# Performance work log

Hardware: AMD Instinct MI355X
Metric: run time of the kernel (lower is better)

Reference implementation:

```python
import jax, jax.numpy as jnp
import numpy as np

NUM_HEADS = 8
NSCALE = 2  # len(sr_ratio) + 1 with sr_ratio=[2.0]


def setup_inputs() -> dict:
    key = jax.random.key(0)
    ks = jax.random.split(key, 12)
    B, Nq, Np, C, n_up, N_all = 16, 1024, 1024, 512, 2048, 4096
    s = C ** -0.5  # keep attention logits in a sane range
    return {
        "query": jax.random.normal(ks[0], (Nq, B, C), jnp.float32),
        "key": jax.random.normal(ks[1], (Np, B, C), jnp.float32),
        "key_pos": jax.random.uniform(ks[2], (B, Np, 3), jnp.float32),
        "xyz_all": jax.random.uniform(ks[3], (B, N_all, 3), jnp.float32),
        "xyz_upsample": jax.random.uniform(ks[4], (B, n_up, 3), jnp.float32),
        "Wq": jax.random.normal(ks[5], (C, C), jnp.float32) * s,
        "Wkv1": jax.random.normal(ks[6], (C, C), jnp.float32) * s,
        "Wkv2": jax.random.normal(ks[7], (C, C), jnp.float32) * s,
        "fp_w": jax.random.normal(ks[8], (C, C), jnp.float32) * s,
        "fp_b": jnp.zeros((C,), jnp.float32),
        "proj_w": jax.random.normal(ks[9], (C, C), jnp.float32) * s,
        "proj_b": jnp.zeros((C,), jnp.float32),
    }


def _fp_upsample(xyz_up, key_pos, key_feats, fp_w, fp_b):
    """PointnetFPModuleUpSample: 3-NN inverse-distance feature interpolation
    from Np known points (key_pos) onto n_up target points, followed by a
    pointwise MLP (1x1 conv, BN folded) + ReLU.
    key_feats: (Np, B, C) -> returns (B, n_up, C)."""
    d2 = jnp.sum((xyz_up[:, :, None, :] - key_pos[:, None, :, :]) ** 2, axis=-1)  # (B, n, Np)
    negd, idx = jax.lax.top_k(-d2, 3)  # 3 nearest neighbors, (B, n, 3)
    w = 1.0 / (-negd + 1e-8)
    w = w / jnp.sum(w, axis=-1, keepdims=True)
    feats = jnp.transpose(key_feats, (1, 0, 2))  # (B, Np, C)
    g = jnp.take_along_axis(feats[:, None, :, :], idx[..., None], axis=2)  # (B, n, 3, C)
    interp = jnp.sum(g * w[..., None], axis=2)  # (B, n, C)
    return jax.nn.relu(interp @ fp_w.T + fp_b)


def reference(query, key, key_pos, xyz_all, xyz_upsample,
              Wq, Wkv1, Wkv2, fp_w, fp_b, proj_w, proj_b):
    Np, B, C = key.shape
    Nq = query.shape[0]
    H = NUM_HEADS
    nh = H // NSCALE  # heads per scale group
    hd = C // H
    scale = hd ** -0.5

    # NOTE: torch reshapes (N,B,C) -> (B,N,...) WITHOUT permuting first; we
    # replicate the identical row-major reshape for bit-faithful structure.
    q = (query @ Wq.T).reshape(B, Nq, H, hd).transpose(0, 2, 1, 3)  # (B,H,Nq,hd)

    def attend(qs, kv):
        k, v = kv[0], kv[1]
        a = jax.nn.softmax(jnp.einsum('bhqd,bhkd->bhqk', qs, k) * scale, axis=-1)
        o = jnp.einsum('bhqk,bhkd->bhqd', a, v)
        return o.transpose(0, 2, 1, 3).reshape(B, Nq, nh * hd)

    # scale 1: full-resolution keys
    kv1 = (key @ Wkv1.T).reshape(B, -1, 2, nh, hd).transpose(2, 0, 3, 1, 4)
    x1 = attend(q[:, :nh], kv1)

    # scale 2: FP-upsampled keys (sr_ratio=2.0 -> 2*base_np points)
    key2 = _fp_upsample(xyz_upsample, key_pos, key, fp_w, fp_b)  # (B, n, C)
    key2_nbc = key2.transpose(1, 0, 2)  # (n, B, C), matches permute(2,0,1) of (B,C,n)
    kv2 = (key2_nbc @ Wkv2.T).reshape(B, -1, 2, nh, hd).transpose(2, 0, 3, 1, 4)
    x2 = attend(q[:, nh:], kv2)

    x = jnp.concatenate([x1, x2], axis=-1) @ proj_w.T + proj_b  # (B, Nq, C)
    return x.transpose(1, 0, 2)  # (Nq, B, C)
```

## Files before the change

### kernel.cpp

```cpp
#include <hip/hip_runtime.h>
#include <cstdint>
#include <cstddef>

#define CD   512
#define BDIM 16
#define NQ   1024
#define NP   1024
#define NUP  2048

typedef unsigned short u16;
typedef short short8 __attribute__((ext_vector_type(8)));
typedef float f32x4  __attribute__((ext_vector_type(4)));
typedef float f32x16 __attribute__((ext_vector_type(16)));
typedef uint32_t u32x4 __attribute__((ext_vector_type(4)));

#define GLOAD16(g, l) __builtin_amdgcn_global_load_lds( \
    (const __attribute__((address_space(1))) void*)(g), \
    (__attribute__((address_space(3))) void*)(l), 16, 0, 0)

__device__ __forceinline__ u16 rne_bf16(float x) {
  uint32_t u = __float_as_uint(x);
  return (u16)((u + 0x7fffu + ((u >> 16) & 1u)) >> 16);
}
__device__ __forceinline__ float bf2f(u16 v) {
  return __uint_as_float(((uint32_t)v) << 16);
}

__global__ __launch_bounds__(256) void prep_kernel(
    const float* __restrict__ query, u16* __restrict__ Qa,
    const float* __restrict__ key, u16* __restrict__ Ka,
    const float* __restrict__ Wq, const float* __restrict__ Wkv1,
    const float* __restrict__ projw, const float* __restrict__ fpw,
    const float* __restrict__ wkv2, u16* __restrict__ Wq2,
    u16* __restrict__ Wkv12, u16* __restrict__ proj2,
    u16* __restrict__ fpwb, u16* __restrict__ wkv2b,
    const float* __restrict__ key_pos, const float* __restrict__ xyz_up,
    int* __restrict__ idx_out, float* __restrict__ w_out)
{
  const int bx = blockIdx.x;
  const int tid = threadIdx.x;
  if (bx < 8832) {
    const float* in; u16* out; float scl = 1.0f; long u;
    if (bx < 8192) {
      in = (bx < 4096) ? query : key;
      out = (bx < 4096) ? Qa : Ka;
      u = (long)(bx & 4095) * 256 + tid;
    } else {
      const int job = (bx - 8192) >> 7;
      in  = (job == 0) ? Wq  : (job == 1) ? Wkv1  : (job == 2) ? projw : (job == 3) ? fpw  : wkv2;
      out = (job == 0) ? Wq2 : (job == 1) ? Wkv12 : (job == 2) ? proj2 : (job == 3) ? fpwb : wkv2b;
      if (job == 0) scl = 0.18033688011112042f;
      u = (long)((bx - 8192) & 127) * 256 + tid;
    }
    const float* ip = in + u * 8;
    float v[8];
    *(float4*)&v[0] = *(const float4*)ip;
    *(float4*)&v[4] = *(const float4*)(ip + 4);
    short8 o;
#pragma unroll
    for (int i = 0; i < 8; ++i) o[i] = (short)rne_bf16(v[i] * scl);
    *(short8*)(out + u * 8) = o;
    return;
  }
  __shared__ __align__(16) float4 kp4[NP];
  const int kb = bx - 8832;
  const int b = kb >> 7;
  const int n0 = (kb & 127) * 16;
  const float* kpb = key_pos + (long)b * NP * 3;
#pragma unroll
  for (int s = 0; s < 4; ++s) {
    const int t = s * 256 + tid;
    kp4[t] = make_float4(kpb[t * 3], kpb[t * 3 + 1], kpb[t * 3 + 2], 0.0f);
  }
  __syncthreads();
  const int sc = tid & 15, pt = tid >> 4;
  const int n = n0 + pt;
  const float ux = xyz_up[(b * NUP + n) * 3 + 0];
  const float uy = xyz_up[(b * NUP + n) * 3 + 1];
  const float uz = xyz_up[(b * NUP + n) * 3 + 2];
  float e0 = 3.4e38f, e1 = 3.4e38f, e2 = 3.4e38f;
  int j0 = 0, j1 = 0, j2 = 0;
  for (int it = 0; it < 64; ++it) {
    const int j = it * 16 + sc;
    const float4 kv = kp4[j];
    const float dx = ux - kv.x, dy = uy - kv.y, dz = uz - kv.z;
    const float dd = dx * dx + dy * dy + dz * dz;
    if (dd < e2) {
      if (dd < e1) {
        e2 = e1; j2 = j1;
        if (dd < e0) { e1 = e0; j1 = j0; e0 = dd; j0 = j; }
        else         { e1 = dd; j1 = j; }
      } else { e2 = dd; j2 = j; }
    }
  }
#pragma unroll
  for (int ms = 1; ms <= 8; ms <<= 1) {
    const float pd0 = __shfl_xor(e0, ms), pd1 = __shfl_xor(e1, ms), pd2 = __shfl_xor(e2, ms);
    const int   pi0 = __shfl_xor(j0, ms), pi1 = __shfl_xor(j1, ms), pi2 = __shfl_xor(j2, ms);
    float cd[3] = {pd0, pd1, pd2};
    int   ci[3] = {pi0, pi1, pi2};
#pragma unroll
    for (int t = 0; t < 3; ++t) {
      const float dd = cd[t]; const int jj = ci[t];
      if (dd < e2 || (dd == e2 && jj < j2)) {
        if (dd < e1 || (dd == e1 && jj < j1)) {
          e2 = e1; j2 = j1;
          if (dd < e0 || (dd == e0 && jj < j0)) { e1 = e0; j1 = j0; e0 = dd; j0 = jj; }
          else                                  { e1 = dd; j1 = jj; }
        } else { e2 = dd; j2 = jj; }
      }
    }
  }
  if (sc == 0) {
    const float w0 = 1.0f / (e0 + 1e-8f);
    const float w1 = 1.0f / (e1 + 1e-8f);
    const float w2 = 1.0f / (e2 + 1e-8f);
    const float inv = 1.0f / ((w0 + w1) + w2);
    const long r = (long)b * NUP + n;
    idx_out[r * 3 + 0] = j0; idx_out[r * 3 + 1] = j1; idx_out[r * 3 + 2] = j2;
    w_out[r * 3 + 0] = w0 * inv; w_out[r * 3 + 1] = w1 * inv; w_out[r * 3 + 2] = w2 * inv;
  }
}

template<int AMODE, int OMODE, int KE, int NKT>
__device__ __forceinline__ void gemm_body64(
    u16* __restrict__ As, u16* __restrict__ Ws,
    const u16* __restrict__ A, const u16* __restrict__ W,
    const float* __restrict__ bias, void* __restrict__ outv,
    u16* __restrict__ Vt, const int m0, const int n0)
{
  const int tid = threadIdx.x;
  const int lane = tid & 63, wv = tid >> 6;
  const int rch = tid & 7;

  f32x4 acc[4][4];
#pragma unroll
  for (int mi = 0; mi < 4; ++mi)
#pragma unroll
    for (int ni = 0; ni < 4; ++ni)
#pragma unroll
      for (int r = 0; r < 4; ++r) acc[mi][ni][r] = 0.0f;

  const long rowb = (long)KE * 2;
  const char* gA[4]; const char* gW[4];
#pragma unroll
  for (int s = 0; s < 4; ++s) {
    const int row = s * 32 + (tid >> 3);
    const int gm = m0 + row;
    const long arow = (AMODE == 0) ? (long)gm : (long)(gm & 15) * 2048 + (gm >> 4);
    const int kb0 = (rch ^ (row & 7)) << 4;
    gA[s] = (const char*)A + arow * rowb + kb0;
    gW[s] = (const char*)W + (long)(n0 + row) * rowb + kb0;
  }
  const int wr = (wv >> 1) * 64, wc = (wv & 1) * 64;
  const int g = lane >> 4, cl = lane & 15;

  for (int kt = 0; kt < KE / 64; ++kt) {
#pragma unroll
    for (int s = 0; s < 4; ++s) {
      GLOAD16(gA[s], (char*)As + (s * 256 + tid) * 16);
      GLOAD16(gW[s], (char*)Ws + (s * 256 + tid) * 16);
      gA[s] += 128; gW[s] += 128;
    }
    __syncthreads();
#pragma unroll
    for (int kb = 0; kb < 2; ++kb) {
      short8 af[4], bf[4];
#pragma unroll
      for (int i = 0; i < 4; ++i) {
        const int ra = wr + i * 16 + cl;
        af[i] = *(const short8*)((const char*)As + ra * 128
                 + ((kb * 64 + g * 16) ^ ((ra & 7) << 4)));
        const int rb = wc + i * 16 + cl;
        bf[i] = *(const short8*)((const char*)Ws + rb * 128
                 + ((kb * 64 + g * 16) ^ ((rb & 7) << 4)));
      }
#pragma unroll
      for (int mi = 0; mi < 4; ++mi)
#pragma unroll
        for (int ni = 0; ni < 4; ++ni)
          acc[mi][ni] = __builtin_amdgcn_mfma_f32_16x16x32_bf16(af[mi], bf[ni], acc[mi][ni], 0, 0, 0);
    }
    __syncthreads();
  }

  if constexpr (OMODE == 3) {
    u16* T = As;
#pragma unroll
    for (int ni = 0; ni < 4; ++ni) {
      const int n = wc + ni * 16 + cl;
      const int swz = (n & 15) << 4;
      const int rb2 = n * 256;
#pragma unroll
      for (int mi = 0; mi < 4; ++mi) {
        uint32_t lo, hi;
        asm("v_cvt_pk_bf16_f32 %0, %1, %2" : "=v"(lo) : "v"(acc[mi][ni][0]), "v"(acc[mi][ni][1]));
        asm("v_cvt_pk_bf16_f32 %0, %1, %2" : "=v"(hi) : "v"(acc[mi][ni][2]), "v"(acc[mi][ni][3]));
        const int m2 = 2 * (wr + mi * 16 + g * 4);
        uint2 pk; pk.x = lo; pk.y = hi;
        *(uint2*)((char*)T + rb2 + (m2 ^ swz)) = pk;
      }
    }
    __syncthreads();
    const int nl = tid >> 1, mh = tid & 1;
    const int v = (n0 - 256) + nl;
    const int hh = v >> 6, dd = v & 63;
    const int bq = m0 / NKT;
    const int p0 = (m0 & (NKT - 1)) + mh * 64;
    u16* dst = Vt + ((size_t)((bq * 4 + hh) * 64 + dd)) * NKT + p0;
    const int swz = (nl & 15) << 4;
#pragma unroll
    for (int j = 0; j < 8; ++j) {
      const int m2 = mh * 128 + j * 16;
      const short8 val = *(const short8*)((const char*)T + nl * 256 + (m2 ^ swz));
      *(short8*)(dst + j * 8) = val;
    }
    return;
  } else {
#pragma unroll
    for (int mi = 0; mi < 4; ++mi)
#pragma unroll
      for (int ni = 0; ni < 4; ++ni)
#pragma unroll
        for (int r = 0; r < 4; ++r) {
          const int gm = m0 + wr + mi * 16 + g * 4 + r;
          const int gn = n0 + wc + ni * 16 + cl;
          float vv = acc[mi][ni][r];
          if (OMODE == 0) {
            ((u16*)outv)[(long)gm * 512 + gn] = rne_bf16(vv);
          } else if (OMODE == 1) {
            vv = fmaxf(vv + bias[gn], 0.0f);
            ((u16*)outv)[(long)gm * 512 + gn] = rne_bf16(vv);
          } else {
            vv += bias[gn];
            ((float*)outv)[((long)(gm & 1023) * BDIM + (gm >> 10)) * 512 + gn] = vv;
          }
        }
  }
}

template<int AMODE, int OMODE, int KE>
__global__ __launch_bounds__(256) void gemm_one(
    const u16* __restrict__ A, const u16* __restrict__ W,
    const float* __restrict__ bias, void* __restrict__ outv)
{
  __shared__ __align__(16) u16 SH[16384];
  gemm_body64<AMODE, OMODE, KE, 1024>(SH, SH + 8192, A, W, bias, outv, nullptr,
                                      blockIdx.x * 128, blockIdx.y * 128);
}

__global__ __launch_bounds__(256) void qkv1_interp_kernel(
    const u16* __restrict__ Qa, const u16* __restrict__ Wq2, u16* __restrict__ Qb,
    const u16* __restrict__ Ka, const u16* __restrict__ Wkv12,
    u16* __restrict__ KV1, u16* __restrict__ Vt1,
    const int* __restrict__ idx, const float* __restrict__ w, u16* __restrict__ IN2)
{
  __shared__ __align__(16) u16 SH[16384];
  const int bid = blockIdx.x;
  if (bid < 512) {
    gemm_body64<0, 0, 512, 1024>(SH, SH + 8192, Qa, Wq2, nullptr, Qb, nullptr,
                                 (bid >> 2) * 128, (bid & 3) * 128);
  } else if (bid < 1024) {
    const int t = bid - 512;
    const int n0 = (t & 3) * 128;
    if (n0 >= 256)
      gemm_body64<0, 3, 512, 1024>(SH, SH + 8192, Ka, Wkv12, nullptr, KV1, Vt1,
                                   (t >> 2) * 128, n0);
    else
      gemm_body64<0, 0, 512, 1024>(SH, SH + 8192, Ka, Wkv12, nullptr, KV1, nullptr,
                                   (t >> 2) * 128, n0);
  } else {
    const int t = threadIdx.x;
    const long r = (long)(bid - 1024) * 4 + (t >> 6);
    const int j = t & 63;
    const int b = (int)(r >> 11);
    const int j0 = idx[r * 3 + 0], j1 = idx[r * 3 + 1], j2 = idx[r * 3 + 2];
    const float w0 = w[r * 3 + 0], w1 = w[r * 3 + 1], w2 = w[r * 3 + 2];
    const short8 a0 = *(const short8*)(Ka + ((long)j0 * BDIM + b) * CD + j * 8);
    const short8 a1 = *(const short8*)(Ka + ((long)j1 * BDIM + b) * CD + j * 8);
    const short8 a2 = *(const short8*)(Ka + ((long)j2 * BDIM + b) * CD + j * 8);
    short8 o;
#pragma unroll
    for (int i = 0; i < 8; ++i)
      o[i] = (short)rne_bf16(bf2f((u16)a0[i]) * w0 + bf2f((u16)a1[i]) * w1
                           + bf2f((u16)a2[i]) * w2);
    *(short8*)(IN2 + r * CD + j * 8) = o;
  }
}

__global__ __launch_bounds__(256) void kv2_kernel(
    const u16* __restrict__ KEY2, const u16* __restrict__ wkv2b,
    u16* __restrict__ KV2, u16* __restrict__ Vt2)
{
  __shared__ __align__(16) u16 SH[16384];
  const int t = blockIdx.x;
  const int n0 = (t & 3) * 128;
  if (n0 >= 256)
    gemm_body64<1, 3, 512, 2048>(SH, SH + 8192, KEY2, wkv2b, nullptr, KV2, Vt2,
                                 (t >> 2) * 128, n0);
  else
    gemm_body64<1, 0, 512, 2048>(SH, SH + 8192, KEY2, wkv2b, nullptr, KV2, nullptr,
                                 (t >> 2) * 128, n0);
}

__global__ __launch_bounds__(256) void gemm_proj64_kernel(
    const u16* __restrict__ A, const u16* __restrict__ W,
    const float* __restrict__ bias, float* __restrict__ out)
{
  __shared__ __align__(16) u16 As[64 * 32];
  __shared__ __align__(16) u16 Ws[128 * 32];
  const int tid = threadIdx.x;
  const int lane = tid & 63, wv = tid >> 6;
  const int m0 = blockIdx.x * 64, n0 = blockIdx.y * 128;

  f32x4 acc[2][4];
#pragma unroll
  for (int mi = 0; mi < 2; ++mi)
#pragma unroll
    for (int ni = 0; ni < 4; ++ni)
#pragma unroll
      for (int r = 0; r < 4; ++r) acc[mi][ni][r] = 0.0f;

  const int ar = tid >> 2, ac = tid & 3;
  const char* gA = (const char*)A + (long)(m0 + ar) * 1024 + ((ac ^ (ar & 3)) << 4);
  const char* gW[2];
#pragma unroll
  for (int s = 0; s < 2; ++s) {
    const int rw = s * 64 + ar;
    gW[s] = (const char*)W + (long)(n0 + rw) * 1024 + ((ac ^ (rw & 3)) << 4);
  }
  const int wr = (wv >> 1) * 32, wc = (wv & 1) * 64;
  const int g = lane >> 4, cl = lane & 15;
  const int gx = (g ^ (cl & 3)) << 4;

  for (int kt = 0; kt < 16; ++kt) {
    GLOAD16(gA, (char*)As + tid * 16); gA += 64;
#pragma unroll
    for (int s = 0; s < 2; ++s) {
      GLOAD16(gW[s], (char*)Ws + (s * 256 + tid) * 16); gW[s] += 64;
    }
    __syncthreads();
    short8 af[2], bf[4];
#pragma unroll
    for (int i = 0; i < 2; ++i)
      af[i] = *(const short8*)((const char*)As + (wr + i * 16 + cl) * 64 + gx);
#pragma unroll
    for (int j = 0; j < 4; ++j)
      bf[j] = *(const short8*)((const char*)Ws + (wc + j * 16 + cl) * 64 + gx);
#pragma unroll
    for (int mi = 0; mi < 2; ++mi)
#pragma unroll
      for (int ni = 0; ni < 4; ++ni)
        acc[mi][ni] = __builtin_amdgcn_mfma_f32_16x16x32_bf16(af[mi], bf[ni], acc[mi][ni], 0, 0, 0);
    __syncthreads();
  }

#pragma unroll
  for (int mi = 0; mi < 2; ++mi)
#pragma unroll
    for (int ni = 0; ni < 4; ++ni)
#pragma unroll
      for (int r = 0; r < 4; ++r) {
        const int gm = m0 + wr + mi * 16 + g * 4 + r;
        const int gn = n0 + wc + ni * 16 + cl;
        out[((long)(gm & 1023) * BDIM + (gm >> 10)) * 512 + gn] = acc[mi][ni][r] + bias[gn];
      }
}

template<int NK>
__device__ __forceinline__ void attn_body32(
    u16* __restrict__ Ks, u16* __restrict__ Vs,
    const u16* __restrict__ Q, const u16* __restrict__ KV,
    const u16* __restrict__ Vt, u16* __restrict__ X,
    const int h, const int sc, const int qt, const int b)
{
  const int tid = threadIdx.x;
  const int lane = tid & 63, wv = tid >> 6;
  const int hi = lane >> 5, ql = lane & 31;

  const u16* qptr = Q + ((size_t)(b * 1024 + qt * 128 + wv * 32 + ql)) * 512
                      + (sc * 4 + h) * 64 + hi * 8;
  short8 qf[4];
#pragma unroll
  for (int t = 0; t < 4; ++t) qf[t] = *(const short8*)(qptr + t * 16);

  f32x16 acc0, acc1;
#pragma unroll
  for (int i = 0; i < 16; ++i) { acc0[i] = 0.0f; acc1[i] = 0.0f; }
  float l = 0.0f;

  const char* kB = (const char*)(KV + (size_t)b * NK * 512 + h * 64);
  const char* vB = (const char*)(Vt + (size_t)((b * 4 + h) * 64) * NK);
  uint32_t koffL[4], voffL[4];
#pragma unroll
  for (int s = 0; s < 4; ++s) {
    const int c = s * 256 + tid;
    { const int key = c >> 3, cp = c & 7;
      koffL[s] = key * 1024 + ((cp ^ (key & 7)) << 4); }
    { const int d = c >> 4, cp = c & 15;
      voffL[s] = d * (NK * 2) + ((cp ^ (d & 15)) << 4); }
  }

  const int sel = ((ql >> 2) ^ (ql >> 3)) & 1;
  const int kpi = ql ^ (sel ? 12 : 0);
  int kaddr[4];
#pragma unroll
  for (int t = 0; t < 4; ++t)
    kaddr[t] = kpi * 128 + (((t * 2 + hi) ^ (kpi & 7)) << 4);
  const int vx = ql & 15;

  constexpr int NT = NK / 128;
#define ISSUE_KV(kt_) { \
  const char* kT_ = kB + (size_t)(kt_) * 131072; \
  const char* vT_ = vB + (size_t)(kt_) * 256; \
  _Pragma("unroll") for (int s_ = 0; s_ < 4; ++s_) { \
    GLOAD16(kT_ + koffL[s_], (char*)Ks + (s_ * 256 + tid) * 16); \
    GLOAD16(vT_ + voffL[s_], (char*)Vs + (s_ * 256 + tid) * 16); } }

  ISSUE_KV(0);

  for (int kt = 0; kt < NT; ++kt) {
    asm volatile("s_waitcnt vmcnt(0)" ::: "memory");
    __builtin_amdgcn_s_barrier();
    __builtin_amdgcn_sched_barrier(0);

#pragma unroll
    for (int blk = 0; blk < 4; ++blk) {
      f32x16 sv;
#pragma unroll
      for (int i = 0; i < 16; ++i) sv[i] = 0.0f;
      __builtin_amdgcn_s_setprio(1);
#pragma unroll
      for (int t = 0; t < 4; ++t) {
        const short8 kf = *(const short8*)((const char*)Ks + blk * 4096 + kaddr[t]);
        sv = __builtin_amdgcn_mfma_f32_32x32x16_bf16(kf, qf[t], sv, 0, 0, 0);
      }
      __builtin_amdgcn_s_setprio(0);
#pragma unroll
      for (int i = 0; i < 16; ++i) {
        sv[i] = __builtin_amdgcn_exp2f(sv[i]);
        l += sv[i];
      }
#pragma unroll
      for (int sh = 0; sh < 2; ++sh) {
        u32x4 pw;
        asm("v_cvt_pk_bf16_f32 %0, %1, %2" : "=v"(pw[0]) : "v"(sv[8*sh+0]), "v"(sv[8*sh+1]));
        asm("v_cvt_pk_bf16_f32 %0, %1, %2" : "=v"(pw[1]) : "v"(sv[8*sh+2]), "v"(sv[8*sh+3]));
        asm("v_cvt_pk_bf16_f32 %0, %1, %2" : "=v"(pw[2]) : "v"(sv[8*sh+4]), "v"(sv[8*sh+5]));
        asm("v_cvt_pk_bf16_f32 %0, %1, %2" : "=v"(pw[3]) : "v"(sv[8*sh+6]), "v"(sv[8*sh+7]));
        const short8 pa = __builtin_bit_cast(short8, pw);
        const int step = blk * 2 + sh;
        const int vchunk = ((step * 2 + hi) ^ vx) << 4;
        __builtin_amdgcn_s_setprio(1);
        {
          const short8 vf0 = *(const short8*)((const char*)Vs + ql * 256 + vchunk);
          acc0 = __builtin_amdgcn_mfma_f32_32x32x16_bf16(pa, vf0, acc0, 0, 0, 0);
          const short8 vf1 = *(const short8*)((const char*)Vs + (32 + ql) * 256 + vchunk);
          acc1 = __builtin_amdgcn_mfma_f32_32x32x16_bf16(pa, vf1, acc1, 0, 0, 0);
        }
        __builtin_amdgcn_s_setprio(0);
      }
    }

    asm volatile("s_waitcnt lgkmcnt(0)" ::: "memory");
    __builtin_amdgcn_sched_barrier(0);
    __builtin_amdgcn_s_barrier();
    if (kt + 1 < NT) { ISSUE_KV(kt + 1); }
  }
#undef ISSUE_KV

  l += __shfl_xor(l, 32);
  const float inv = 1.0f / l;
  const long qbase = (long)b * 1024 + qt * 128 + wv * 32;
#pragma unroll
  for (int i = 0; i < 16; ++i) {
    const int row = (i & 3) + 8 * (i >> 2) + 4 * hi;
    const float ir = __shfl(inv, row);
    const long go = (qbase + row) * 512 + sc * 256 + h * 64 + ql;
    X[go]      = rne_bf16(acc0[i] * ir);
    X[go + 32] = rne_bf16(acc1[i] * ir);
  }
}

__global__ __launch_bounds__(256, 4) void attn_fused32_kernel(
    const u16* __restrict__ Q,
    const u16* __restrict__ KV1, const u16* __restrict__ KV2,
    const u16* __restrict__ Vt1, const u16* __restrict__ Vt2,
    u16* __restrict__ X)
{
  __shared__ __align__(16) u16 Ks[128 * 64];
  __shared__ __align__(16) u16 Vs[64 * 128];
  const int d = blockIdx.x;
  const int qt = (d >> 3) & 7;
  const int grp = (d & 7) | ((d >> 6) << 3);
  const int b = grp & 15, z = grp >> 4;
  if (z < 4) attn_body32<1024>(Ks, Vs, Q, KV1, Vt1, X, z, 0, qt, b);
  else       attn_body32<2048>(Ks, Vs, Q, KV2, Vt2, X, z - 4, 1, qt, b);
}

extern "C" void kernel_launch(void* const* d_in, const int* in_sizes, int n_in,
                              void* d_out, int out_size, void* d_ws, size_t ws_size,
                              hipStream_t stream) {
  const float* query   = (const float*)d_in[0];
  const float* key     = (const float*)d_in[1];
  const float* key_pos = (const float*)d_in[2];
  const float* xyz_up  = (const float*)d_in[4];
  const float* Wq      = (const float*)d_in[5];
  const float* Wkv1    = (const float*)d_in[6];
  const float* Wkv2    = (const float*)d_in[7];
  const float* fp_w    = (const float*)d_in[8];
  const float* fp_b    = (const float*)d_in[9];
  const float* proj_w  = (const float*)d_in[10];
  const float* proj_b  = (const float*)d_in[11];

  char* ws = (char*)d_ws;
  const size_t MB = 1024 * 1024;
  u16*  Qa    = (u16*)(ws + 0);
  u16*  Ka    = (u16*)(ws + 16 * MB);
  u16*  Qb    = (u16*)(ws + 32 * MB);
  u16*  KV1   = (u16*)(ws + 48 * MB);
  u16*  IN2   = (u16*)(ws + 64 * MB);
  u16*  KEY2  = (u16*)(ws + 96 * MB);
  u16*  Vt1   = (u16*)(ws + 128 * MB);
  u16*  Vt2   = (u16*)(ws + 136 * MB);
  u16*  Wq2   = (u16*)(ws + 152 * MB);
  u16*  Wkv12 = (u16*)(ws + 152 * MB + 512 * 1024);
  u16*  proj2 = (u16*)(ws + 153 * MB);
  u16*  fpwb  = (u16*)(ws + 153 * MB + 512 * 1024);
  u16*  wkv2b = (u16*)(ws + 154 * MB);
  int*  idxb  = (int*)(ws + 155 * MB);
  float* wb   = (float*)(ws + 156 * MB);
  u16*  KV2   = IN2;
  u16*  X     = Qa;

  prep_kernel<<<dim3(10880), 256, 0, stream>>>(
      query, Qa, key, Ka, Wq, Wkv1, proj_w, fp_w, Wkv2,
      Wq2, Wkv12, proj2, fpwb, wkv2b, key_pos, xyz_up, idxb, wb);
  qkv1_interp_kernel<<<dim3(9216), 256, 0, stream>>>(
      Qa, Wq2, Qb, Ka, Wkv12, KV1, Vt1, idxb, wb, IN2);
  gemm_one<0, 1, 512><<<dim3(256, 4), 256, 0, stream>>>(IN2, fpwb, fp_b, KEY2);
  kv2_kernel<<<dim3(1024), 256, 0, stream>>>(KEY2, wkv2b, KV2, Vt2);
  attn_fused32_kernel<<<dim3(1024), 256, 0, stream>>>(Qb, KV1, KV2, Vt1, Vt2, X);
  gemm_proj64_kernel<<<dim3(256, 4), 256, 0, stream>>>(X, proj2, proj_b, (float*)d_out);
}
```

Measured before the change: 236.9 us.

## Double-buffer attention K/V tiles, double query rows per wave, swizzle GEMM blocks

The attention kernel now has each wave handle 64 query rows (two 32-row MFMA tiles), so every K/V fragment loaded from LDS feeds twice as many MFMAs. K/V tiles are double-buffered in 64KB of LDS, with the next tile's global loads issued before the current tile is computed, which removes the trailing barrier. Occupancy drops to 2 blocks per SM and register pressure rises. All GEMM kernels switch to a 1D grid with a block-index swizzle that groups 8 M-tiles across the 4 N-tiles, aiming for better L2 reuse.

```diff
diff --git a/kernel.cpp b/kernel.cpp
--- a/kernel.cpp
+++ b/kernel.cpp
@@ -239,14 +239,17 @@
   }
 }
 
-template<int AMODE, int OMODE, int KE>
-__global__ __launch_bounds__(256) void gemm_one(
+__device__ __forceinline__ int swz_p(int d)  { return (d & 7) | ((d >> 5) << 3); }
+__device__ __forceinline__ int swz_nt(int d) { return (d >> 3) & 3; }
+
+__global__ __launch_bounds__(256) void gemm_fp_kernel(
     const u16* __restrict__ A, const u16* __restrict__ W,
-    const float* __restrict__ bias, void* __restrict__ outv)
+    const float* __restrict__ bias, u16* __restrict__ outv)
 {
   __shared__ __align__(16) u16 SH[16384];
-  gemm_body64<AMODE, OMODE, KE, 1024>(SH, SH + 8192, A, W, bias, outv, nullptr,
-                                      blockIdx.x * 128, blockIdx.y * 128);
+  const int d = blockIdx.x;
+  gemm_body64<0, 1, 512, 1024>(SH, SH + 8192, A, W, bias, outv, nullptr,
+                               swz_p(d) * 128, swz_nt(d) * 128);
 }
 
 __global__ __launch_bounds__(256) void qkv1_interp_kernel(
@@ -259,16 +262,16 @@
   const int bid = blockIdx.x;
   if (bid < 512) {
     gemm_body64<0, 0, 512, 1024>(SH, SH + 8192, Qa, Wq2, nullptr, Qb, nullptr,
-                                 (bid >> 2) * 128, (bid & 3) * 128);
+                                 swz_p(bid) * 128, swz_nt(bid) * 128);
   } else if (bid < 1024) {
     const int t = bid - 512;
-    const int n0 = (t & 3) * 128;
+    const int n0 = swz_nt(t) * 128;
     if (n0 >= 256)
       gemm_body64<0, 3, 512, 1024>(SH, SH + 8192, Ka, Wkv12, nullptr, KV1, Vt1,
-                                   (t >> 2) * 128, n0);
+                                   swz_p(t) * 128, n0);
     else
       gemm_body64<0, 0, 512, 1024>(SH, SH + 8192, Ka, Wkv12, nullptr, KV1, nullptr,
-                                   (t >> 2) * 128, n0);
+                                   swz_p(t) * 128, n0);
   } else {
     const int t = threadIdx.x;
     const long r = (long)(bid - 1024) * 4 + (t >> 6);
@@ -293,14 +296,14 @@
     u16* __restrict__ KV2, u16* __restrict__ Vt2)
 {
   __shared__ __align__(16) u16 SH[16384];
-  const int t = blockIdx.x;
-  const int n0 = (t & 3) * 128;
+  const int d = blockIdx.x;
+  const int n0 = swz_nt(d) * 128;
   if (n0 >= 256)
     gemm_body64<1, 3, 512, 2048>(SH, SH + 8192, KEY2, wkv2b, nullptr, KV2, Vt2,
-                                 (t >> 2) * 128, n0);
+                                 swz_p(d) * 128, n0);
   else
     gemm_body64<1, 0, 512, 2048>(SH, SH + 8192, KEY2, wkv2b, nullptr, KV2, nullptr,
-                                 (t >> 2) * 128, n0);
+                                 swz_p(d) * 128, n0);
 }
 
 __global__ __launch_bounds__(256) void gemm_proj64_kernel(
@@ -311,7 +314,8 @@
   __shared__ __align__(16) u16 Ws[128 * 32];
   const int tid = threadIdx.x;
   const int lane = tid & 63, wv = tid >> 6;
-  const int m0 = blockIdx.x * 64, n0 = blockIdx.y * 128;
+  const int d = blockIdx.x;
+  const int m0 = swz_p(d) * 64, n0 = swz_nt(d) * 128;
 
   f32x4 acc[2][4];
 #pragma unroll
@@ -368,8 +372,8 @@
 }
 
 template<int NK>
-__device__ __forceinline__ void attn_body32(
-    u16* __restrict__ Ks, u16* __restrict__ Vs,
+__device__ __forceinline__ void attn_body32d(
+    u16* __restrict__ SH,
     const u16* __restrict__ Q, const u16* __restrict__ KV,
     const u16* __restrict__ Vt, u16* __restrict__ X,
     const int h, const int sc, const int qt, const int b)
@@ -378,16 +382,20 @@
   const int lane = tid & 63, wv = tid >> 6;
   const int hi = lane >> 5, ql = lane & 31;
 
-  const u16* qptr = Q + ((size_t)(b * 1024 + qt * 128 + wv * 32 + ql)) * 512
-                      + (sc * 4 + h) * 64 + hi * 8;
-  short8 qf[4];
-#pragma unroll
-  for (int t = 0; t < 4; ++t) qf[t] = *(const short8*)(qptr + t * 16);
-
-  f32x16 acc0, acc1;
-#pragma unroll
-  for (int i = 0; i < 16; ++i) { acc0[i] = 0.0f; acc1[i] = 0.0f; }
-  float l = 0.0f;
+  const long qbase = (long)b * 1024 + qt * 256 + wv * 64;
+  const u16* qpA = Q + (qbase + ql) * 512 + (sc * 4 + h) * 64 + hi * 8;
+  const u16* qpB = qpA + 32 * 512;
+  short8 qfA[4], qfB[4];
+#pragma unroll
+  for (int t = 0; t < 4; ++t) {
+    qfA[t] = *(const short8*)(qpA + t * 16);
+    qfB[t] = *(const short8*)(qpB + t * 16);
+  }
+
+  f32x16 aA0, aA1, aB0, aB1;
+#pragma unroll
+  for (int i = 0; i < 16; ++i) { aA0[i] = 0.f; aA1[i] = 0.f; aB0[i] = 0.f; aB1[i] = 0.f; }
+  float lA = 0.0f, lB = 0.0f;
 
   const char* kB = (const char*)(KV + (size_t)b * NK * 512 + h * 64);
   const char* vB = (const char*)(Vt + (size_t)((b * 4 + h) * 64) * NK);
@@ -397,8 +405,8 @@
     const int c = s * 256 + tid;
     { const int key = c >> 3, cp = c & 7;
       koffL[s] = key * 1024 + ((cp ^ (key & 7)) << 4); }
-    { const int d = c >> 4, cp = c & 15;
-      voffL[s] = d * (NK * 2) + ((cp ^ (d & 15)) << 4); }
+    { const int dd = c >> 4, cp = c & 15;
+      voffL[s] = dd * (NK * 2) + ((cp ^ (dd & 15)) << 4); }
   }
 
   const int sel = ((ql >> 2) ^ (ql >> 3)) & 1;
@@ -410,92 +418,104 @@
   const int vx = ql & 15;
 
   constexpr int NT = NK / 128;
-#define ISSUE_KV(kt_) { \
+#define ISSUE_KV(kt_, bo_) { \
   const char* kT_ = kB + (size_t)(kt_) * 131072; \
   const char* vT_ = vB + (size_t)(kt_) * 256; \
   _Pragma("unroll") for (int s_ = 0; s_ < 4; ++s_) { \
-    GLOAD16(kT_ + koffL[s_], (char*)Ks + (s_ * 256 + tid) * 16); \
-    GLOAD16(vT_ + voffL[s_], (char*)Vs + (s_ * 256 + tid) * 16); } }
-
-  ISSUE_KV(0);
+    GLOAD16(kT_ + koffL[s_], (char*)SH + (bo_) + (s_ * 256 + tid) * 16); \
+    GLOAD16(vT_ + voffL[s_], (char*)SH + (bo_) + 16384 + (s_ * 256 + tid) * 16); } }
+
+  int bo = 0;
+  ISSUE_KV(0, 0);
 
   for (int kt = 0; kt < NT; ++kt) {
     asm volatile("s_waitcnt vmcnt(0)" ::: "memory");
     __builtin_amdgcn_s_barrier();
     __builtin_amdgcn_sched_barrier(0);
+    if (kt + 1 < NT) { ISSUE_KV(kt + 1, bo ^ 32768); }
+
+    const char* Ksb = (const char*)SH + bo;
+    const char* Vsb = Ksb + 16384;
 
 #pragma unroll
     for (int blk = 0; blk < 4; ++blk) {
-      f32x16 sv;
-#pragma unroll
-      for (int i = 0; i < 16; ++i) sv[i] = 0.0f;
+      f32x16 svA, svB;
+#pragma unroll
+      for (int i = 0; i < 16; ++i) { svA[i] = 0.f; svB[i] = 0.f; }
       __builtin_amdgcn_s_setprio(1);
 #pragma unroll
       for (int t = 0; t < 4; ++t) {
-        const short8 kf = *(const short8*)((const char*)Ks + blk * 4096 + kaddr[t]);
-        sv = __builtin_amdgcn_mfma_f32_32x32x16_bf16(kf, qf[t], sv, 0, 0, 0);
+        const short8 kf = *(const short8*)(Ksb + blk * 4096 + kaddr[t]);
+        svA = __builtin_amdgcn_mfma_f32_32x32x16_bf16(kf, qfA[t], svA, 0, 0, 0);
+        svB = __builtin_amdgcn_mfma_f32_32x32x16_bf16(kf, qfB[t], svB, 0, 0, 0);
       }
       __builtin_amdgcn_s_setprio(0);
 #pragma unroll
       for (int i = 0; i < 16; ++i) {
-        sv[i] = __builtin_amdgcn_exp2f(sv[i]);
-        l += sv[i];
+        svA[i] = __builtin_amdgcn_exp2f(svA[i]); lA += svA[i];
+        svB[i] = __builtin_amdgcn_exp2f(svB[i]); lB += svB[i];
       }
 #pragma unroll
       for (int sh = 0; sh < 2; ++sh) {
-        u32x4 pw;
-        asm("v_cvt_pk_bf16_f32 %0, %1, %2" : "=v"(pw[0]) : "v"(sv[8*sh+0]), "v"(sv[8*sh+1]));
-        asm("v_cvt_pk_bf16_f32 %0, %1, %2" : "=v"(pw[1]) : "v"(sv[8*sh+2]), "v"(sv[8*sh+3]));
-        asm("v_cvt_pk_bf16_f32 %0, %1, %2" : "=v"(pw[2]) : "v"(sv[8*sh+4]), "v"(sv[8*sh+5]));
-        asm("v_cvt_pk_bf16_f32 %0, %1, %2" : "=v"(pw[3]) : "v"(sv[8*sh+6]), "v"(sv[8*sh+7]));
-        const short8 pa = __builtin_bit_cast(short8, pw);
-        const int step = blk * 2 + sh;
-        const int vchunk = ((step * 2 + hi) ^ vx) << 4;
+        u32x4 pwA, pwB;
+        asm("v_cvt_pk_bf16_f32 %0, %1, %2" : "=v"(pwA[0]) : "v"(svA[8*sh+0]), "v"(svA[8*sh+1]));
+        asm("v_cvt_pk_bf16_f32 %0, %1, %2" : "=v"(pwA[1]) : "v"(svA[8*sh+2]), "v"(svA[8*sh+3]));
+        asm("v_cvt_pk_bf16_f32 %0, %1, %2" : "=v"(pwA[2]) : "v"(svA[8*sh+4]), "v"(svA[8*sh+5]));
+        asm("v_cvt_pk_bf16_f32 %0, %1, %2" : "=v"(pwA[3]) : "v"(svA[8*sh+6]), "v"(svA[8*sh+7]));
+        asm("v_cvt_pk_bf16_f32 %0, %1, %2" : "=v"(pwB[0]) : "v"(svB[8*sh+0]), "v"(svB[8*sh+1]));
+        asm("v_cvt_pk_bf16_f32 %0, %1, %2" : "=v"(pwB[1]) : "v"(svB[8*sh+2]), "v"(svB[8*sh+3]));
+        asm("v_cvt_pk_bf16_f32 %0, %1, %2" : "=v"(pwB[2]) : "v"(svB[8*sh+4]), "v"(svB[8*sh+5]));
+        asm("v_cvt_pk_bf16_f32 %0, %1, %2" : "=v"(pwB[3]) : "v"(svB[8*sh+6]), "v"(svB[8*sh+7]));
+        const short8 paA = __builtin_bit_cast(short8, pwA);
+        const short8 paB = __builtin_bit_cast(short8, pwB);
+        const int vchunk = (((blk * 2 + sh) * 2 + hi) ^ vx) << 4;
         __builtin_amdgcn_s_setprio(1);
         {
-          const short8 vf0 = *(const short8*)((const char*)Vs + ql * 256 + vchunk);
-          acc0 = __builtin_amdgcn_mfma_f32_32x32x16_bf16(pa, vf0, acc0, 0, 0, 0);
-          const short8 vf1 = *(const short8*)((const char*)Vs + (32 + ql) * 256 + vchunk);
-          acc1 = __builtin_amdgcn_mfma_f32_32x32x16_bf16(pa, vf1, acc1, 0, 0, 0);
+          const short8 vf0 = *(const short8*)(Vsb + ql * 256 + vchunk);
+          const short8 vf1 = *(const short8*)(Vsb + (32 + ql) * 256 + vchunk);
+          aA0 = __builtin_amdgcn_mfma_f32_32x32x16_bf16(paA, vf0, aA0, 0, 0, 0);
+          aA1 = __builtin_amdgcn_mfma_f32_32x32x16_bf16(paA, vf1, aA1, 0, 0, 0);
+          aB0 = __builtin_amdgcn_mfma_f32_32x32x16_bf16(paB, vf0, aB0, 0, 0, 0);
+          aB1 = __builtin_amdgcn_mfma_f32_32x32x16_bf16(paB, vf1, aB1, 0, 0, 0);
         }
         __builtin_amdgcn_s_setprio(0);
       }
     }
-
-    asm volatile("s_waitcnt lgkmcnt(0)" ::: "memory");
-    __builtin_amdgcn_sched_barrier(0);
-    __builtin_amdgcn_s_barrier();
-    if (kt + 1 < NT) { ISSUE_KV(kt + 1); }
+    bo ^= 32768;
   }
 #undef ISSUE_KV
 
-  l += __shfl_xor(l, 32);
-  const float inv = 1.0f / l;
-  const long qbase = (long)b * 1024 + qt * 128 + wv * 32;
+  lA += __shfl_xor(lA, 32);
+  lB += __shfl_xor(lB, 32);
+  const float invA = 1.0f / lA;
+  const float invB = 1.0f / lB;
 #pragma unroll
   for (int i = 0; i < 16; ++i) {
     const int row = (i & 3) + 8 * (i >> 2) + 4 * hi;
-    const float ir = __shfl(inv, row);
-    const long go = (qbase + row) * 512 + sc * 256 + h * 64 + ql;
-    X[go]      = rne_bf16(acc0[i] * ir);
-    X[go + 32] = rne_bf16(acc1[i] * ir);
-  }
-}
-
-__global__ __launch_bounds__(256, 4) void attn_fused32_kernel(
+    const float irA = __shfl(invA, row);
+    const float irB = __shfl(invB, row);
+    const long goA = (qbase + row) * 512 + sc * 256 + h * 64 + ql;
+    const long goB = (qbase + 32 + row) * 512 + sc * 256 + h * 64 + ql;
+    X[goA]      = rne_bf16(aA0[i] * irA);
+    X[goA + 32] = rne_bf16(aA1[i] * irA);
+    X[goB]      = rne_bf16(aB0[i] * irB);
+    X[goB + 32] = rne_bf16(aB1[i] * irB);
+  }
+}
+
+__global__ __launch_bounds__(256, 2) void attn_fused32_kernel(
     const u16* __restrict__ Q,
     const u16* __restrict__ KV1, const u16* __restrict__ KV2,
     const u16* __restrict__ Vt1, const u16* __restrict__ Vt2,
     u16* __restrict__ X)
 {
-  __shared__ __align__(16) u16 Ks[128 * 64];
-  __shared__ __align__(16) u16 Vs[64 * 128];
+  __shared__ __align__(16) u16 SH[32768];
   const int d = blockIdx.x;
-  const int qt = (d >> 3) & 7;
-  const int grp = (d & 7) | ((d >> 6) << 3);
+  const int qt = (d >> 3) & 3;
+  const int grp = (d & 7) | ((d >> 5) << 3);
   const int b = grp & 15, z = grp >> 4;
-  if (z < 4) attn_body32<1024>(Ks, Vs, Q, KV1, Vt1, X, z, 0, qt, b);
-  else       attn_body32<2048>(Ks, Vs, Q, KV2, Vt2, X, z - 4, 1, qt, b);
+  if (z < 4) attn_body32d<1024>(SH, Q, KV1, Vt1, X, z, 0, qt, b);
+  else       attn_body32d<2048>(SH, Q, KV2, Vt2, X, z - 4, 1, qt, b);
 }
 
 extern "C" void kernel_launch(void* const* d_in, const int* in_sizes, int n_in,
@@ -538,8 +558,8 @@
       Wq2, Wkv12, proj2, fpwb, wkv2b, key_pos, xyz_up, idxb, wb);
   qkv1_interp_kernel<<<dim3(9216), 256, 0, stream>>>(
       Qa, Wq2, Qb, Ka, Wkv12, KV1, Vt1, idxb, wb, IN2);
-  gemm_one<0, 1, 512><<<dim3(256, 4), 256, 0, stream>>>(IN2, fpwb, fp_b, KEY2);
+  gemm_fp_kernel<<<dim3(1024), 256, 0, stream>>>(IN2, fpwb, fp_b, KEY2);
   kv2_kernel<<<dim3(1024), 256, 0, stream>>>(KEY2, wkv2b, KV2, Vt2);
-  attn_fused32_kernel<<<dim3(1024), 256, 0, stream>>>(Qb, KV1, KV2, Vt1, Vt2, X);
-  gemm_proj64_kernel<<<dim3(256, 4), 256, 0, stream>>>(X, proj2, proj_b, (float*)d_out);
-}
+  attn_fused32_kernel<<<dim3(512), 256, 0, stream>>>(Qb, KV1, KV2, Vt1, Vt2, X);
+  gemm_proj64_kernel<<<dim3(1024), 256, 0, stream>>>(X, proj2, proj_b, (float*)d_out);
+}
```

After: 210.9 us. 11.0% less time.
